# Kernel tuning notes

Measured on AMD Instinct MI355X. Metric: run time of the kernel, lower is better.

The kernel has to match this reference:

```python
import jax, jax.numpy as jnp
import numpy as np

B, S, H, I, E, R = 2, 2048, 4096, 11008, 4, 8
SCALE = 16.0 / 8.0  # lora_alpha / rank


def _lora(x, A, Bm):
    # x:[N,in], A:[R,in], Bm:[out,R] -> [N,out]
    return (x @ A.T) @ Bm.T * SCALE


def _tmoe(x, router, A, Bm):
    # dense softmax routing over E experts, each a rank-R LoRA
    gates = jax.nn.softmax(x @ router.T, axis=-1)          # [N,E]
    a = jnp.einsum('nh,erh->ner', x, A)                    # [N,E,R]
    return jnp.einsum('ne,ner,eor->no', gates, a, Bm) * SCALE


def _delta(xf, mask, vA, vB, router, tA, tB):
    # image tokens -> V-Adapter LoRA, text tokens -> T-MoE (kd_mode=False)
    return jnp.where(mask[:, None], _lora(xf, vA, vB), _tmoe(xf, router, tA, tB))


def setup_inputs() -> dict:
    key = jax.random.key(0)
    ks = jax.random.split(key, 21)
    w = lambda k, shape: jax.random.normal(k, shape, dtype=jnp.float32) * 0.02
    return {
        'x': jax.random.normal(ks[0], (B, S, H), dtype=jnp.float32) * 0.5,
        'image_mask': jax.random.randint(ks[1], (B, S), 0, 2) == 1,
        'Wg': w(ks[2], (I, H)), 'Wu': w(ks[3], (I, H)), 'Wd': w(ks[4], (H, I)),
        'va_gate_A': w(ks[5], (R, H)), 'va_gate_B': w(ks[6], (I, R)),
        'va_up_A': w(ks[7], (R, H)), 'va_up_B': w(ks[8], (I, R)),
        'va_down_A': w(ks[9], (R, I)), 'va_down_B': w(ks[10], (H, R)),
        'router_gate': w(ks[11], (E, H)), 'tm_gate_A': w(ks[12], (E, R, H)), 'tm_gate_B': w(ks[13], (E, I, R)),
        'router_up': w(ks[14], (E, H)), 'tm_up_A': w(ks[15], (E, R, H)), 'tm_up_B': w(ks[16], (E, I, R)),
        'router_down': w(ks[17], (E, I)), 'tm_down_A': w(ks[18], (E, R, I)), 'tm_down_B': w(ks[19], (E, H, R)),
    }


def reference(x, image_mask, Wg, Wu, Wd,
              va_gate_A, va_gate_B, va_up_A, va_up_B, va_down_A, va_down_B,
              router_gate, tm_gate_A, tm_gate_B,
              router_up, tm_up_A, tm_up_B,
              router_down, tm_down_A, tm_down_B):
    Bb, Ss, Hh = x.shape
    xf = x.reshape(-1, Hh)                                  # [N,H]
    m = image_mask.reshape(-1)                              # [N]
    gate = xf @ Wg.T + _delta(xf, m, va_gate_A, va_gate_B, router_gate, tm_gate_A, tm_gate_B)
    up = xf @ Wu.T + _delta(xf, m, va_up_A, va_up_B, router_up, tm_up_A, tm_up_B)
    inter = jax.nn.silu(gate) * up                          # [N,I]
    out = inter @ Wd.T + _delta(inter, m, va_down_A, va_down_B, router_down, tm_down_A, tm_down_B)
    return out.reshape(Bb, Ss, Hh)
```

## Files before the change

### kernel.cpp

```cpp
#include <hip/hip_runtime.h>
#include <hip/hip_bf16.h>
#include <stdint.h>


#define H_DIM 4096
#define I_DIM 11008
#define N_TOK 4096
#define R_RANK 8
#define K1P 4224
#define K2P 11136

typedef __attribute__((ext_vector_type(8))) __bf16 bf16x8;
typedef __attribute__((ext_vector_type(4))) __bf16 bf16x4;
typedef __attribute__((ext_vector_type(4))) float  f32x4;

__device__ __forceinline__ void gload16(const void* g, const void* lds_wave_base) {
  auto gp = (const __attribute__((address_space(1))) void*)(uintptr_t)g;
  auto lp = (__attribute__((address_space(3))) void*)(uintptr_t)lds_wave_base;
  __builtin_amdgcn_global_load_lds(gp, lp, 16, 0, 0);
}

#define BAR()    asm volatile("s_barrier" ::: "memory")
#define LGKM0()  do { asm volatile("s_waitcnt lgkmcnt(0)" ::: "memory"); \
                      __builtin_amdgcn_sched_barrier(0); } while (0)
#define SCHEDB() __builtin_amdgcn_sched_barrier(0)

__device__ __forceinline__ void detect_mask(const void* mask, int t, int* okI, int* okF) {
  const unsigned int* mi = (const unsigned int*)mask;
  int bad_i = 0, bad_f = 0;
  for (int idx = t; idx < 1024; idx += 256) {
    unsigned v = mi[idx];
    bad_i |= !(v == 0u || v == 1u);
    bad_f |= !(v == 0u || v == 0x3f800000u);
  }
  if (bad_i) *okI = 0;
  if (bad_f) *okF = 0;
}
__device__ __forceinline__ bool read_mask(const void* mask, int n, int okI, int okF) {
  if (okI) return ((const int*)mask)[n] != 0;
  if (okF) return ((const float*)mask)[n] != 0.0f;
  return ((const unsigned char*)mask)[n] != 0;
}

__global__ __launch_bounds__(256)
void prepAll(const float* __restrict__ Wg, const float* __restrict__ Wu,
             const float* __restrict__ Wd,
             const float* __restrict__ vBg, const float* __restrict__ tmBg,
             const float* __restrict__ vBu, const float* __restrict__ tmBu,
             const float* __restrict__ vBd, const float* __restrict__ tmBd,
             const float* __restrict__ vAg, const float* __restrict__ tmAg, const float* __restrict__ rg,
             const float* __restrict__ vAu, const float* __restrict__ tmAu, const float* __restrict__ ru,
             const float* __restrict__ vAd, const float* __restrict__ tmAd, const float* __restrict__ rd,
             __bf16* __restrict__ Wcat, __bf16* __restrict__ Wda,
             __bf16* __restrict__ W88b, __bf16* __restrict__ W44b) {
  int b = blockIdx.x, t = threadIdx.x;
  if (b < I_DIM) {
    int i = b;
    int grp = i >> 7, within = i & 127;
    const float4* g4 = (const float4*)(Wg + (size_t)i * H_DIM);
    const float4* u4 = (const float4*)(Wu + (size_t)i * H_DIM);
    __bf16* og = Wcat + (size_t)(grp * 256 + within) * K1P;
    __bf16* ou = Wcat + (size_t)(grp * 256 + 128 + within) * K1P;
    for (int c = t; c < H_DIM / 4; c += 256) {
      float4 v = g4[c];
      bf16x4 bb = {(__bf16)v.x, (__bf16)v.y, (__bf16)v.z, (__bf16)v.w};
      *(bf16x4*)(og + c * 4) = bb;
      v = u4[c];
      bf16x4 b2 = {(__bf16)v.x, (__bf16)v.y, (__bf16)v.z, (__bf16)v.w};
      *(bf16x4*)(ou + c * 4) = b2;
    }
    if (t < 128) {
      float gv = 0.f, uv = 0.f;
      if (t < 8) gv = 2.f * vBg[i * R_RANK + t];
      else if (t < 40) { int e = (t - 8) >> 3, r = (t - 8) & 7;
        gv = 2.f * tmBg[((size_t)e * I_DIM + i) * R_RANK + r]; }
      if (t >= 40 && t < 48) uv = 2.f * vBu[i * R_RANK + (t - 40)];
      else if (t >= 48 && t < 80) { int e = (t - 48) >> 3, r = (t - 48) & 7;
        uv = 2.f * tmBu[((size_t)e * I_DIM + i) * R_RANK + r]; }
      og[H_DIM + t] = (__bf16)gv;
      ou[H_DIM + t] = (__bf16)uv;
    }
  } else if (b < I_DIM + 88) {
    int r = b - I_DIM;
    const float* src;
    if      (r <  8) src = vAg  + (size_t)r * H_DIM;
    else if (r < 40) src = tmAg + (size_t)(r - 8) * H_DIM;
    else if (r < 44) src = rg   + (size_t)(r - 40) * H_DIM;
    else if (r < 52) src = vAu  + (size_t)(r - 44) * H_DIM;
    else if (r < 84) src = tmAu + (size_t)(r - 52) * H_DIM;
    else             src = ru   + (size_t)(r - 84) * H_DIM;
    __bf16* dst = W88b + (size_t)r * H_DIM;
    for (int c = t; c < H_DIM / 4; c += 256) {
      float4 v = ((const float4*)src)[c];
      bf16x4 bb = {(__bf16)v.x, (__bf16)v.y, (__bf16)v.z, (__bf16)v.w};
      *(bf16x4*)(dst + c * 4) = bb;
    }
  } else if (b < I_DIM + 132) {
    int r = b - I_DIM - 88;
    const float* src = (r < 8)  ? vAd  + (size_t)r * I_DIM
                     : (r < 40) ? tmAd + (size_t)(r - 8) * I_DIM
                                : rd   + (size_t)(r - 40) * I_DIM;
    __bf16* dst = W44b + (size_t)r * I_DIM;
    for (int c = t; c < I_DIM / 4; c += 256) {
      float4 v = ((const float4*)src)[c];
      bf16x4 bb = {(__bf16)v.x, (__bf16)v.y, (__bf16)v.z, (__bf16)v.w};
      *(bf16x4*)(dst + c * 4) = bb;
    }
  } else {
    int o = b - I_DIM - 132;
    const float4* w4 = (const float4*)(Wd + (size_t)o * I_DIM);
    __bf16* orow = Wda + (size_t)o * K2P;
    for (int c = t; c < I_DIM / 4; c += 256) {
      float4 v = w4[c];
      bf16x4 bb = {(__bf16)v.x, (__bf16)v.y, (__bf16)v.z, (__bf16)v.w};
      *(bf16x4*)(orow + c * 4) = bb;
    }
    if (t < 128) {
      float v = 0.f;
      if (t < 8) v = 2.f * vBd[o * R_RANK + t];
      else if (t < 40) { int e = (t - 8) >> 3, r = (t - 8) & 7;
        v = 2.f * tmBd[((size_t)e * H_DIM + o) * R_RANK + r]; }
      orow[I_DIM + t] = (__bf16)v;
    }
  }
}

__global__ __launch_bounds__(256)
void prep_x(const float* __restrict__ x, const void* __restrict__ mask,
            const __bf16* __restrict__ W88b, __bf16* __restrict__ Xaug) {
  __shared__ __align__(16) float sx[4][H_DIM];
  __shared__ float dots[4][88];
  __shared__ int okI, okF;
  int t = threadIdx.x, n0 = blockIdx.x * 4;
  if (t == 0) { okI = 1; okF = 1; }
  __syncthreads();
  detect_mask(mask, t, &okI, &okF);
  for (int tok = 0; tok < 4; ++tok) {
    const float4* xr = (const float4*)(x + (size_t)(n0 + tok) * H_DIM);
    __bf16* orow = Xaug + (size_t)(n0 + tok) * K1P;
    for (int c = t; c < H_DIM / 4; c += 256) {
      float4 v = xr[c];
      *(float4*)&sx[tok][c * 4] = v;
      bf16x4 b = {(__bf16)v.x, (__bf16)v.y, (__bf16)v.z, (__bf16)v.w};
      *(bf16x4*)(orow + c * 4) = b;
    }
  }
  __syncthreads();
  int wv = t >> 6, ln = t & 63;
  for (int gi = 0; gi < 6; ++gi) {
    int g = wv + gi * 4;
    if (g >= 22) break;
    int i0 = g * 4;
    const __bf16* base = W88b + (size_t)i0 * H_DIM;
    float acc[4][4];
#pragma unroll
    for (int ii = 0; ii < 4; ++ii)
#pragma unroll
      for (int tk = 0; tk < 4; ++tk) acc[ii][tk] = 0.f;
    for (int j = 0; j < H_DIM / 256; ++j) {
      int h = j * 256 + ln * 4;
      float4 v0 = *(const float4*)&sx[0][h];
      float4 v1 = *(const float4*)&sx[1][h];
      float4 v2 = *(const float4*)&sx[2][h];
      float4 v3 = *(const float4*)&sx[3][h];
#pragma unroll
      for (int ii = 0; ii < 4; ++ii) {
        bf16x4 wb = *(const bf16x4*)(base + (size_t)ii * H_DIM + h);
        float wx = (float)wb[0], wy = (float)wb[1], wz = (float)wb[2], ww = (float)wb[3];
        acc[ii][0] = fmaf(v0.x, wx, fmaf(v0.y, wy, fmaf(v0.z, wz, fmaf(v0.w, ww, acc[ii][0]))));
        acc[ii][1] = fmaf(v1.x, wx, fmaf(v1.y, wy, fmaf(v1.z, wz, fmaf(v1.w, ww, acc[ii][1]))));
        acc[ii][2] = fmaf(v2.x, wx, fmaf(v2.y, wy, fmaf(v2.z, wz, fmaf(v2.w, ww, acc[ii][2]))));
        acc[ii][3] = fmaf(v3.x, wx, fmaf(v3.y, wy, fmaf(v3.z, wz, fmaf(v3.w, ww, acc[ii][3]))));
      }
    }
#pragma unroll
    for (int ii = 0; ii < 4; ++ii) {
#pragma unroll
      for (int tk = 0; tk < 4; ++tk) {
        float a = acc[ii][tk];
        for (int s = 32; s > 0; s >>= 1) a += __shfl_xor(a, s);
        if (ln == 0) dots[tk][i0 + ii] = a;
      }
    }
  }
  __syncthreads();
  for (int pass = 0; pass < 2; ++pass) {
    int tok = (t >> 7) + pass * 2;
    int s = t & 127;
    const float* dd = dots[tok];
    bool img = read_mask(mask, n0 + tok, okI, okF);
    float c = 0.f;
    if (s < 80) {
      if (s < 40) {
        if (img) { if (s < 8) c = dd[s]; }
        else if (s >= 8) {
          float l0 = dd[40], l1 = dd[41], l2 = dd[42], l3 = dd[43];
          float mx = fmaxf(fmaxf(l0, l1), fmaxf(l2, l3));
          float e0 = __expf(l0 - mx), e1 = __expf(l1 - mx), e2 = __expf(l2 - mx), e3 = __expf(l3 - mx);
          float inv = 1.f / (e0 + e1 + e2 + e3);
          int e = (s - 8) >> 3;
          float ge = (e == 0 ? e0 : e == 1 ? e1 : e == 2 ? e2 : e3) * inv;
          c = ge * dd[s];
        }
      } else {
        int s2 = s - 40;
        if (img) { if (s2 < 8) c = dd[44 + s2]; }
        else if (s2 >= 8) {
          float l0 = dd[84], l1 = dd[85], l2 = dd[86], l3 = dd[87];
          float mx = fmaxf(fmaxf(l0, l1), fmaxf(l2, l3));
          float e0 = __expf(l0 - mx), e1 = __expf(l1 - mx), e2 = __expf(l2 - mx), e3 = __expf(l3 - mx);
          float inv = 1.f / (e0 + e1 + e2 + e3);
          int e = (s2 - 8) >> 3;
          float ge = (e == 0 ? e0 : e == 1 ? e1 : e == 2 ? e2 : e3) * inv;
          c = ge * dd[44 + s2];
        }
      }
    }
    Xaug[(size_t)(n0 + tok) * K1P + H_DIM + s] = (__bf16)c;
  }
}

__global__ __launch_bounds__(512)
void prep_x2(const void* __restrict__ mask, const __bf16* __restrict__ W44b,
             __bf16* __restrict__ X2) {
  __shared__ __align__(16) __bf16 si[2][I_DIM];
  __shared__ float dots[2][44];
  __shared__ int okI, okF;
  int t = threadIdx.x, n0 = blockIdx.x * 2;
  if (t == 0) { okI = 1; okF = 1; }
  __syncthreads();
  if (t < 256) detect_mask(mask, t, &okI, &okF);
  for (int tok = 0; tok < 2; ++tok) {
    const bf16x8* xr = (const bf16x8*)(X2 + (size_t)(n0 + tok) * K2P);
    bf16x8* srow = (bf16x8*)&si[tok][0];
    for (int c = t; c < I_DIM / 8; c += 512) srow[c] = xr[c];
  }
  __syncthreads();
  int wv = t >> 6, ln = t & 63;
  const bf16x8* s0 = (const bf16x8*)&si[0][0];
  const bf16x8* s1 = (const bf16x8*)&si[1][0];
  for (int gi = 0; gi < 2; ++gi) {
    int g = wv + gi * 8;
    if (g >= 11) break;
    int i0 = g * 4;
    const __bf16* base = W44b + (size_t)i0 * I_DIM;
    float acc[4][2];
#pragma unroll
    for (int ii = 0; ii < 4; ++ii) { acc[ii][0] = 0.f; acc[ii][1] = 0.f; }
    for (int j = 0; j < 22; ++j) {
      int ch = j * 64 + ln;
      if (ch < I_DIM / 8) {
        bf16x8 x0 = s0[ch], x1 = s1[ch];
        float xf0[8], xf1[8];
#pragma unroll
        for (int k = 0; k < 8; ++k) { xf0[k] = (float)x0[k]; xf1[k] = (float)x1[k]; }
#pragma unroll
        for (int ii = 0; ii < 4; ++ii) {
          bf16x8 wv8 = *(const bf16x8*)(base + (size_t)ii * I_DIM + ch * 8);
          float a0 = acc[ii][0], a1 = acc[ii][1];
#pragma unroll
          for (int k = 0; k < 8; ++k) {
            float wk = (float)wv8[k];
            a0 = fmaf(xf0[k], wk, a0);
            a1 = fmaf(xf1[k], wk, a1);
          }
          acc[ii][0] = a0; acc[ii][1] = a1;
        }
      }
    }
#pragma unroll
    for (int ii = 0; ii < 4; ++ii) {
#pragma unroll
      for (int tk = 0; tk < 2; ++tk) {
        float a = acc[ii][tk];
        for (int s = 32; s > 0; s >>= 1) a += __shfl_xor(a, s);
        if (ln == 0) dots[tk][i0 + ii] = a;
      }
    }
  }
  __syncthreads();
  if (t < 256) {
    int tok = t >> 7, s = t & 127;
    const float* dd = dots[tok];
    bool img = read_mask(mask, n0 + tok, okI, okF);
    float c = 0.f;
    if (s < 40) {
      if (img) { if (s < 8) c = dd[s]; }
      else if (s >= 8) {
        float l0 = dd[40], l1 = dd[41], l2 = dd[42], l3 = dd[43];
        float mx = fmaxf(fmaxf(l0, l1), fmaxf(l2, l3));
        float e0 = __expf(l0 - mx), e1 = __expf(l1 - mx), e2 = __expf(l2 - mx), e3 = __expf(l3 - mx);
        float inv = 1.f / (e0 + e1 + e2 + e3);
        int e = (s - 8) >> 3;
        float ge = (e == 0 ? e0 : e == 1 ? e1 : e == 2 ? e2 : e3) * inv;
        c = ge * dd[s];
      }
    }
    X2[(size_t)(n0 + tok) * K2P + I_DIM + s] = (__bf16)c;
  }
}

template<int MH, int NH>
__device__ __forceinline__ void mfmaq(f32x4 (&acc)[8][4], const bf16x8 (&av)[4][2],
                                      const bf16x8 (&bv)[2][2]) {
#pragma unroll
  for (int kk = 0; kk < 2; ++kk)
#pragma unroll
    for (int j = 0; j < 2; ++j)
#pragma unroll
      for (int i = 0; i < 4; ++i)
        acc[MH * 4 + i][NH * 2 + j] = __builtin_amdgcn_mfma_f32_16x16x32_bf16(
            av[i][kk], bv[j][kk], acc[MH * 4 + i][NH * 2 + j], 0, 0, 0);
}

template<int KS, int NT, int GN, typename OutT, int OSTR, int EPI, int MODE>
__global__ __launch_bounds__(512, 2)
void gemm256(const __bf16* __restrict__ A, const __bf16* __restrict__ Bm,
             OutT* __restrict__ C) {
  __shared__ __align__(16) char lds[131072];

  int t = threadIdx.x;
  int w = t >> 6, l = t & 63;
  int wm = w >> 2, wn = w & 3;
  int lrow = l & 15, kq = l >> 4;

  int nwg = gridDim.x, bid = blockIdx.x;
  int tm, tn;
  if constexpr (MODE == 1) {
    int xx = bid & 7, ii = bid >> 3;
    tm = ((xx & 1) << 3) | (ii & 7);
    tn = ((xx >> 1) << 2) | (ii >> 3);
  } else if constexpr (MODE == 2) {
    constexpr int FULL = (GN / 16) * 256;
    if (bid < FULL) { int s = bid >> 8, ww = bid & 255; tm = ww & 15; tn = s * 16 + (ww >> 4); }
    else            { int ww = bid - FULL; tm = ww & 15; tn = (GN / 16) * 16 + (ww >> 4); }
  } else {
    int swz = (bid & 7) * (nwg >> 3) + (bid >> 3);
    tm = swz / GN; tn = swz % GN;
  }
  int m0 = tm * 256, n0 = tn * 256;

  int grow = (t >> 3) & 7;
  int gcole = ((t & 7) ^ grow) << 3;
  const __bf16* gA0 = A  + (size_t)(m0 + w * 8 + grow) * KS + gcole;
  const __bf16* gB0 = Bm + (size_t)(n0 + w * 8 + grow) * KS + gcole;
  char* ldsA0 = lds + w * 1024;
  char* ldsB0 = lds + 32768 + w * 1024;

  auto stageA = [&](int buf, int tt, int c) {
    gload16(gA0 + (size_t)c * (64 * KS) + (size_t)tt * 64,
            ldsA0 + buf * 65536 + c * 8192);
  };
  auto stageB = [&](int buf, int tt, int c) {
    gload16(gB0 + (size_t)c * (64 * KS) + (size_t)tt * 64,
            ldsB0 + buf * 65536 + c * 8192);
  };

  int aBase = (wm * 128 + lrow) * 128;
  int bBase = (wn * 64 + lrow) * 128;
  int sw    = (lrow & 7) << 4;
  int col0  = (kq * 16) ^ sw;
  int col1  = (64 + kq * 16) ^ sw;

  f32x4 acc[8][4];
#pragma unroll
  for (int i = 0; i < 8; ++i)
#pragma unroll
    for (int j = 0; j < 4; ++j) acc[i][j] = (f32x4){0.f, 0.f, 0.f, 0.f};

#pragma unroll
  for (int c = 0; c < 4; ++c) { stageA(0, 0, c); stageB(0, 0, c); }
#pragma unroll
  for (int c = 0; c < 4; ++c) { stageA(1, 1, c); stageB(1, 1, c); }
  asm volatile("s_waitcnt vmcnt(8)" ::: "memory");
  BAR();

  bf16x8 b0v[2][2];
  {
    const char* sb0 = lds + 32768;
#pragma unroll
    for (int j = 0; j < 2; ++j) {
      b0v[j][0] = *(const bf16x8*)(sb0 + bBase + j * 2048 + col0);
      b0v[j][1] = *(const bf16x8*)(sb0 + bBase + j * 2048 + col1);
    }
  }

  int cur = 0;
  for (int tt = 0; tt < NT; ++tt, cur ^= 1) {
    const char* sa  = lds + (cur ? 65536 : 0);
    const char* sb  = sa + 32768;
    const char* sbN = lds + (cur ? 0 : 65536) + 32768;
    int t2 = tt + 2;
    bool st   = t2 < NT;
    bool more = tt + 1 < NT;
    bf16x8 aF[4][2], b1v[2][2];

#pragma unroll
    for (int i = 0; i < 4; ++i) {
      aF[i][0] = *(const bf16x8*)(sa + aBase + i * 2048 + col0);
      aF[i][1] = *(const bf16x8*)(sa + aBase + i * 2048 + col1);
    }
    BAR(); LGKM0();
    __builtin_amdgcn_s_setprio(1);
    mfmaq<0, 0>(acc, aF, b0v);
    __builtin_amdgcn_s_setprio(0);
    BAR();

    if (st) { stageA(cur, t2, 0); stageA(cur, t2, 2); }
#pragma unroll
    for (int j = 0; j < 2; ++j) {
      b1v[j][0] = *(const bf16x8*)(sb + bBase + (2 + j) * 2048 + col0);
      b1v[j][1] = *(const bf16x8*)(sb + bBase + (2 + j) * 2048 + col1);
    }
    BAR(); LGKM0();
    __builtin_amdgcn_s_setprio(1);
    mfmaq<0, 1>(acc, aF, b1v);
    __builtin_amdgcn_s_setprio(0);
    BAR();

    if (st) { stageB(cur, t2, 0); stageB(cur, t2, 1); }
#pragma unroll
    for (int i = 0; i < 4; ++i) {
      aF[i][0] = *(const bf16x8*)(sa + aBase + (4 + i) * 2048 + col0);
      aF[i][1] = *(const bf16x8*)(sa + aBase + (4 + i) * 2048 + col1);
    }
    BAR(); LGKM0();
    __builtin_amdgcn_s_setprio(1);
    mfmaq<1, 0>(acc, aF, b0v);
    __builtin_amdgcn_s_setprio(0);
    BAR();

    if (st) { stageB(cur, t2, 2); stageB(cur, t2, 3);
              stageA(cur, t2, 1); stageA(cur, t2, 3); }
    if (st) asm volatile("s_waitcnt vmcnt(8)" ::: "memory");
    else    asm volatile("s_waitcnt vmcnt(0)" ::: "memory");
    SCHEDB();
    if (more) {
#pragma unroll
      for (int j = 0; j < 2; ++j) {
        b0v[j][0] = *(const bf16x8*)(sbN + bBase + j * 2048 + col0);
        b0v[j][1] = *(const bf16x8*)(sbN + bBase + j * 2048 + col1);
      }
    }
    __builtin_amdgcn_s_setprio(1);
    mfmaq<1, 1>(acc, aF, b1v);
    __builtin_amdgcn_s_setprio(0);
    BAR();
  }

  if constexpr (EPI == 0) {
    int r0 = m0 + wm * 128 + kq * 4;
    int c0 = n0 + wn * 64 + lrow;
#pragma unroll
    for (int mi = 0; mi < 8; ++mi) {
#pragma unroll
      for (int q = 0; q < 4; ++q) {
        OutT* p = C + (size_t)(r0 + mi * 16 + q) * OSTR + c0;
#pragma unroll
        for (int ni = 0; ni < 4; ++ni) p[ni * 16] = (OutT)acc[mi][ni][q];
      }
    }
  } else {
    float* xch = (float*)lds;
    bool isGate = (wn < 2);
    int p = wm * 2 + (wn & 1);
    float* mybuf = xch + (size_t)p * 8192 + (isGate ? 4096 : 0);
#pragma unroll
    for (int mi = 0; mi < 4; ++mi) {
      int msrc = isGate ? (4 + mi) : mi;
#pragma unroll
      for (int q = 0; q < 4; ++q) {
        int r = mi * 16 + kq * 4 + q;
        int key = (r >> 2) & 3;
#pragma unroll
        for (int ni = 0; ni < 4; ++ni) {
          int c = (ni * 16 + lrow) ^ (key << 4);
          mybuf[r * 64 + c] = acc[msrc][ni][q];
        }
      }
    }
    __syncthreads();
    const float* pbuf = xch + (size_t)p * 8192 + (isGate ? 0 : 4096);
    int mbase = isGate ? 0 : 4;
    int rowoff = isGate ? 0 : 64;
#pragma unroll
    for (int mi = 0; mi < 4; ++mi) {
#pragma unroll
      for (int q = 0; q < 4; ++q) {
        int r = mi * 16 + kq * 4 + q;
        int key = (r >> 2) & 3;
        int row = m0 + wm * 128 + rowoff + r;
        OutT* orow = C + (size_t)row * OSTR + tn * 128 + (wn & 1) * 64 + lrow;
#pragma unroll
        for (int ni = 0; ni < 4; ++ni) {
          int c = (ni * 16 + lrow) ^ (key << 4);
          float o = pbuf[r * 64 + c];
          float g = isGate ? acc[mbase + mi][ni][q] : o;
          float u = isGate ? o : acc[mbase + mi][ni][q];
          orow[ni * 16] = (OutT)(g / (1.f + __expf(-g)) * u);
        }
      }
    }
  }
}

extern "C" void kernel_launch(void* const* d_in, const int* in_sizes, int n_in,
                              void* d_out, int out_size, void* d_ws, size_t ws_size,
                              hipStream_t stream) {
  const float* x    = (const float*)d_in[0];
  const void*  mask = d_in[1];
  const float* Wg   = (const float*)d_in[2];
  const float* Wu   = (const float*)d_in[3];
  const float* Wd   = (const float*)d_in[4];
  const float* vAg  = (const float*)d_in[5];
  const float* vBg  = (const float*)d_in[6];
  const float* vAu  = (const float*)d_in[7];
  const float* vBu  = (const float*)d_in[8];
  const float* vAd  = (const float*)d_in[9];
  const float* vBd  = (const float*)d_in[10];
  const float* rg   = (const float*)d_in[11];
  const float* tmAg = (const float*)d_in[12];
  const float* tmBg = (const float*)d_in[13];
  const float* ru   = (const float*)d_in[14];
  const float* tmAu = (const float*)d_in[15];
  const float* tmBu = (const float*)d_in[16];
  const float* rd   = (const float*)d_in[17];
  const float* tmAd = (const float*)d_in[18];
  const float* tmBd = (const float*)d_in[19];

  char* ws = (char*)d_ws;
  __bf16* Xaug = (__bf16*)(ws);
  __bf16* Wcat = (__bf16*)(ws + 34603008);
  __bf16* X2   = (__bf16*)(ws + 220594176);
  __bf16* Wda  = (__bf16*)(ws + 311820288);
  __bf16* W88b = (__bf16*)d_out;
  __bf16* W44b = (__bf16*)((char*)d_out + 1048576);

  prepAll<<<I_DIM + 132 + H_DIM, 256, 0, stream>>>(
      Wg, Wu, Wd, vBg, tmBg, vBu, tmBu, vBd, tmBd,
      vAg, tmAg, rg, vAu, tmAu, ru, vAd, tmAd, rd,
      Wcat, Wda, W88b, W44b);
  prep_x<<<N_TOK / 4, 256, 0, stream>>>(x, mask, W88b, Xaug);

  gemm256<K1P, K1P / 64, 86, __bf16, K2P, 1, 2>
      <<<(N_TOK / 256) * 86, 512, 0, stream>>>(Xaug, Wcat, X2);

  prep_x2<<<N_TOK / 2, 512, 0, stream>>>(mask, W44b, X2);

  gemm256<K2P, K2P / 64, H_DIM / 256, float, H_DIM, 0, 1>
      <<<(N_TOK / 256) * (H_DIM / 256), 512, 0, stream>>>(X2, Wda, (float*)d_out);
}
```

Measured before the change: 1.418 ms.

## Prefetch LDS fragments earlier in GEMM loop and process 4 tokens per prep_x2 block

The GEMM main loop now issues the LDS reads for the next sub-step's B and second-half A fragments right after the wait, before the current MFMA batch, using a separate aH register set, so LDS latency overlaps with matrix math. prep_x2 handles four tokens per block instead of two, reusing each loaded W44b row across more tokens and halving the block count. The changes raise register pressure in the GEMM (an extra 8 bf16x8 fragments) and LDS use in prep_x2 (about 88KB), which could lower occupancy or cause spills.

```diff
diff --git a/kernel.cpp b/kernel.cpp
--- a/kernel.cpp
+++ b/kernel.cpp
@@ -223,14 +223,14 @@
 __global__ __launch_bounds__(512)
 void prep_x2(const void* __restrict__ mask, const __bf16* __restrict__ W44b,
              __bf16* __restrict__ X2) {
-  __shared__ __align__(16) __bf16 si[2][I_DIM];
-  __shared__ float dots[2][44];
+  __shared__ __align__(16) __bf16 si[4][I_DIM];
+  __shared__ float dots[4][44];
   __shared__ int okI, okF;
-  int t = threadIdx.x, n0 = blockIdx.x * 2;
+  int t = threadIdx.x, n0 = blockIdx.x * 4;
   if (t == 0) { okI = 1; okF = 1; }
   __syncthreads();
   if (t < 256) detect_mask(mask, t, &okI, &okF);
-  for (int tok = 0; tok < 2; ++tok) {
+  for (int tok = 0; tok < 4; ++tok) {
     const bf16x8* xr = (const bf16x8*)(X2 + (size_t)(n0 + tok) * K2P);
     bf16x8* srow = (bf16x8*)&si[tok][0];
     for (int c = t; c < I_DIM / 8; c += 512) srow[c] = xr[c];
@@ -239,39 +239,48 @@
   int wv = t >> 6, ln = t & 63;
   const bf16x8* s0 = (const bf16x8*)&si[0][0];
   const bf16x8* s1 = (const bf16x8*)&si[1][0];
+  const bf16x8* s2 = (const bf16x8*)&si[2][0];
+  const bf16x8* s3 = (const bf16x8*)&si[3][0];
   for (int gi = 0; gi < 2; ++gi) {
     int g = wv + gi * 8;
     if (g >= 11) break;
     int i0 = g * 4;
     const __bf16* base = W44b + (size_t)i0 * I_DIM;
-    float acc[4][2];
-#pragma unroll
-    for (int ii = 0; ii < 4; ++ii) { acc[ii][0] = 0.f; acc[ii][1] = 0.f; }
+    float acc[4][4];
+#pragma unroll
+    for (int ii = 0; ii < 4; ++ii)
+#pragma unroll
+      for (int tk = 0; tk < 4; ++tk) acc[ii][tk] = 0.f;
     for (int j = 0; j < 22; ++j) {
       int ch = j * 64 + ln;
       if (ch < I_DIM / 8) {
-        bf16x8 x0 = s0[ch], x1 = s1[ch];
-        float xf0[8], xf1[8];
-#pragma unroll
-        for (int k = 0; k < 8; ++k) { xf0[k] = (float)x0[k]; xf1[k] = (float)x1[k]; }
+        bf16x8 x0 = s0[ch], x1 = s1[ch], x2 = s2[ch], x3 = s3[ch];
+        float xf0[8], xf1[8], xf2[8], xf3[8];
+#pragma unroll
+        for (int k = 0; k < 8; ++k) {
+          xf0[k] = (float)x0[k]; xf1[k] = (float)x1[k];
+          xf2[k] = (float)x2[k]; xf3[k] = (float)x3[k];
+        }
 #pragma unroll
         for (int ii = 0; ii < 4; ++ii) {
           bf16x8 wv8 = *(const bf16x8*)(base + (size_t)ii * I_DIM + ch * 8);
-          float a0 = acc[ii][0], a1 = acc[ii][1];
+          float a0 = acc[ii][0], a1 = acc[ii][1], a2 = acc[ii][2], a3 = acc[ii][3];
 #pragma unroll
           for (int k = 0; k < 8; ++k) {
             float wk = (float)wv8[k];
             a0 = fmaf(xf0[k], wk, a0);
             a1 = fmaf(xf1[k], wk, a1);
+            a2 = fmaf(xf2[k], wk, a2);
+            a3 = fmaf(xf3[k], wk, a3);
           }
-          acc[ii][0] = a0; acc[ii][1] = a1;
+          acc[ii][0] = a0; acc[ii][1] = a1; acc[ii][2] = a2; acc[ii][3] = a3;
         }
       }
     }
 #pragma unroll
     for (int ii = 0; ii < 4; ++ii) {
 #pragma unroll
-      for (int tk = 0; tk < 2; ++tk) {
+      for (int tk = 0; tk < 4; ++tk) {
         float a = acc[ii][tk];
         for (int s = 32; s > 0; s >>= 1) a += __shfl_xor(a, s);
         if (ln == 0) dots[tk][i0 + ii] = a;
@@ -279,7 +288,7 @@
     }
   }
   __syncthreads();
-  if (t < 256) {
+  {
     int tok = t >> 7, s = t & 127;
     const float* dd = dots[tok];
     bool img = read_mask(mask, n0 + tok, okI, okF);
@@ -393,7 +402,7 @@
     int t2 = tt + 2;
     bool st   = t2 < NT;
     bool more = tt + 1 < NT;
-    bf16x8 aF[4][2], b1v[2][2];
+    bf16x8 aF[4][2], aH[4][2], b1v[2][2];
 
 #pragma unroll
     for (int i = 0; i < 4; ++i) {
@@ -401,32 +410,32 @@
       aF[i][1] = *(const bf16x8*)(sa + aBase + i * 2048 + col1);
     }
     BAR(); LGKM0();
+#pragma unroll
+    for (int j = 0; j < 2; ++j) {
+      b1v[j][0] = *(const bf16x8*)(sb + bBase + (2 + j) * 2048 + col0);
+      b1v[j][1] = *(const bf16x8*)(sb + bBase + (2 + j) * 2048 + col1);
+    }
     __builtin_amdgcn_s_setprio(1);
     mfmaq<0, 0>(acc, aF, b0v);
     __builtin_amdgcn_s_setprio(0);
     BAR();
 
     if (st) { stageA(cur, t2, 0); stageA(cur, t2, 2); }
-#pragma unroll
-    for (int j = 0; j < 2; ++j) {
-      b1v[j][0] = *(const bf16x8*)(sb + bBase + (2 + j) * 2048 + col0);
-      b1v[j][1] = *(const bf16x8*)(sb + bBase + (2 + j) * 2048 + col1);
-    }
     BAR(); LGKM0();
+#pragma unroll
+    for (int i = 0; i < 4; ++i) {
+      aH[i][0] = *(const bf16x8*)(sa + aBase + (4 + i) * 2048 + col0);
+      aH[i][1] = *(const bf16x8*)(sa + aBase + (4 + i) * 2048 + col1);
+    }
     __builtin_amdgcn_s_setprio(1);
     mfmaq<0, 1>(acc, aF, b1v);
     __builtin_amdgcn_s_setprio(0);
     BAR();
 
     if (st) { stageB(cur, t2, 0); stageB(cur, t2, 1); }
-#pragma unroll
-    for (int i = 0; i < 4; ++i) {
-      aF[i][0] = *(const bf16x8*)(sa + aBase + (4 + i) * 2048 + col0);
-      aF[i][1] = *(const bf16x8*)(sa + aBase + (4 + i) * 2048 + col1);
-    }
     BAR(); LGKM0();
     __builtin_amdgcn_s_setprio(1);
-    mfmaq<1, 0>(acc, aF, b0v);
+    mfmaq<1, 0>(acc, aH, b0v);
     __builtin_amdgcn_s_setprio(0);
     BAR();
 
@@ -443,7 +452,7 @@
       }
     }
     __builtin_amdgcn_s_setprio(1);
-    mfmaq<1, 1>(acc, aF, b1v);
+    mfmaq<1, 1>(acc, aH, b1v);
     __builtin_amdgcn_s_setprio(0);
     BAR();
   }
@@ -545,7 +554,7 @@
   gemm256<K1P, K1P / 64, 86, __bf16, K2P, 1, 2>
       <<<(N_TOK / 256) * 86, 512, 0, stream>>>(Xaug, Wcat, X2);
 
-  prep_x2<<<N_TOK / 2, 512, 0, stream>>>(mask, W44b, X2);
+  prep_x2<<<N_TOK / 4, 512, 0, stream>>>(mask, W44b, X2);
 
   gemm256<K2P, K2P / 64, H_DIM / 256, float, H_DIM, 0, 1>
       <<<(N_TOK / 256) * (H_DIM / 256), 512, 0, stream>>>(X2, Wda, (float*)d_out);
```

Result: slower. 1.489 ms (+5.0%).
